# Optimization experiments

Measured on AMD Instinct MI355X. Metric: run time of the kernel, lower is better.

## Reference

```python
import jax, jax.numpy as jnp
import numpy as np

N_NODES = 100000
N_EDGES = 1600000


def spmm(edge_index, edge_vals, x, n_nodes):
    # adj @ x with adj in COO form: out[dst] += val * x[src]
    src = edge_index[0]
    dst = edge_index[1]
    gathered = x[src] * edge_vals[:, None]  # [E, F]
    return jax.ops.segment_sum(gathered, dst, num_segments=n_nodes)


def setup_inputs() -> dict:
    key = jax.random.key(0)
    ks = jax.random.split(key, 8)
    x = jax.random.normal(ks[0], (N_NODES, 512), dtype=jnp.float32)
    edge_index = jax.random.randint(ks[1], (2, N_EDGES), 0, N_NODES, dtype=jnp.int64)
    edge_vals = jax.random.uniform(ks[2], (N_EDGES,), dtype=jnp.float32)
    # xavier-uniform style weights, zero biases (as in initialize_weights)
    def xavier(k, fan_in, fan_out):
        lim = float(np.sqrt(6.0 / (fan_in + fan_out)))
        return jax.random.uniform(k, (fan_in, fan_out), minval=-lim, maxval=lim, dtype=jnp.float32)
    W1 = xavier(ks[3], 512, 128)
    b1 = jnp.zeros((128,), jnp.float32)
    W2 = xavier(ks[4], 128, 64)
    b2 = jnp.zeros((64,), jnp.float32)
    W3 = xavier(ks[5], 64, 16)
    b3 = jnp.zeros((16,), jnp.float32)
    return {"x": x, "edge_index": edge_index, "edge_vals": edge_vals,
            "W1": W1, "b1": b1, "W2": W2, "b2": b2, "W3": W3, "b3": b3}


def reference(x, edge_index, edge_vals, W1, b1, W2, b2, W3, b3):
    n = x.shape[0]
    h = jax.nn.relu(spmm(edge_index, edge_vals, x @ W1 + b1, n))
    h = jax.nn.relu(spmm(edge_index, edge_vals, h @ W2 + b2, n))
    logits = spmm(edge_index, edge_vals, h @ W3 + b3, n)
    logp = jax.nn.log_softmax(logits, axis=1)
    return jnp.argmax(logp, axis=1)
```

## Files before the change

### kernel.cpp

```cpp
#include <hip/hip_runtime.h>

typedef _Float16 half8 __attribute__((ext_vector_type(8)));
typedef float floatx4 __attribute__((ext_vector_type(4)));

#define BSHIFT 7
#define BMASK 127
#define EPB 8192
#define P2CAP 4096

__device__ __forceinline__ void g2lds16(const void* g, void* l) {
    __builtin_amdgcn_global_load_lds(
        (const __attribute__((address_space(1))) void*)(unsigned long long)g,
        (__attribute__((address_space(3))) void*)(unsigned int)(unsigned long long)l,
        16, 0, 0);
}


__global__ __launch_bounds__(256) void p1a_hist(const int* __restrict__ dst,
                                                int* __restrict__ hist,
                                                int E, int NBUCK) {
    extern __shared__ int lh[];
    int b = blockIdx.x, t = threadIdx.x;
    for (int k = t; k < NBUCK; k += 256) lh[k] = 0;
    __syncthreads();
    int e0 = b * EPB;
    int eend = min(e0 + EPB, E);
    for (int i = e0 + t; i < eend; i += 256)
        atomicAdd(&lh[dst[i] >> BSHIFT], 1);
    __syncthreads();
    for (int k = t; k < NBUCK; k += 256) hist[(size_t)b * NBUCK + k] = lh[k];
}

__global__ __launch_bounds__(256) void p1b_scan(const int* __restrict__ hist,
                                                int* __restrict__ blockOff,
                                                int* __restrict__ btot,
                                                int NBLK, int NBUCK) {
    int k = blockIdx.x * 256 + threadIdx.x;
    if (k < NBUCK) {
        int run = 0;
        for (int b = 0; b < NBLK; ++b) {
            int c = hist[(size_t)b * NBUCK + k];
            blockOff[(size_t)b * NBUCK + k] = run;
            run += c;
        }
        btot[k] = run;
    }
}

__global__ __launch_bounds__(1024) void p1c_bscan(const int* __restrict__ btot,
                                                  int* __restrict__ bstart,
                                                  int* __restrict__ rowptr,
                                                  int NBUCK, int M, int E) {
    __shared__ int s[1024];
    int tid = threadIdx.x;
    int v = (tid < NBUCK) ? btot[tid] : 0;
    s[tid] = v;
    __syncthreads();
    for (int off = 1; off < 1024; off <<= 1) {
        int t = (tid >= off) ? s[tid - off] : 0;
        __syncthreads();
        s[tid] += t;
        __syncthreads();
    }
    if (tid < NBUCK) bstart[tid] = s[tid] - v;
    if (tid == 0) rowptr[M] = E;
}

__global__ __launch_bounds__(256) void p1d_scatter(const int* __restrict__ src,
                                                   const int* __restrict__ dst,
                                                   const float* __restrict__ val,
                                                   const int* __restrict__ bstart,
                                                   const int* __restrict__ blockOff,
                                                   int2* __restrict__ tmp,
                                                   int E, int NBUCK) {
    extern __shared__ int cur[];
    int b = blockIdx.x, t = threadIdx.x;
    for (int k = t; k < NBUCK; k += 256)
        cur[k] = bstart[k] + blockOff[(size_t)b * NBUCK + k];
    __syncthreads();
    int e0 = b * EPB;
    int eend = min(e0 + EPB, E);
    for (int i = e0 + t; i < eend; i += 256) {
        int d = dst[i];
        int p = atomicAdd(&cur[d >> BSHIFT], 1);
        int2 pk;
        pk.x = src[i] | ((d & BMASK) << 20);
        pk.y = __float_as_int(val[i]);
        tmp[p] = pk;
    }
}

__global__ __launch_bounds__(256) void p2_sort(const int2* __restrict__ tmp,
                                               const int* __restrict__ bstart,
                                               const int* __restrict__ btot,
                                               int* __restrict__ rowptr,
                                               int2* __restrict__ ssv, int M) {
    __shared__ int2 ebuf[P2CAP];
    __shared__ int h[128], sc[128], curs[128];
    int k = blockIdx.x, t = threadIdx.x;
    int base = bstart[k], n = btot[k];
    for (int j = t; j < 128; j += 256) h[j] = 0;
    __syncthreads();
    int nl = min(n, P2CAP);
    for (int i = t; i < nl; i += 256) {
        int2 e = tmp[base + i];
        ebuf[i] = e;
        atomicAdd(&h[e.x >> 20], 1);
    }
    for (int i = P2CAP + t; i < n; i += 256) {
        int2 e = tmp[base + i];
        atomicAdd(&h[e.x >> 20], 1);
    }
    __syncthreads();
    if (t < 128) sc[t] = h[t];
    __syncthreads();
    for (int off = 1; off < 128; off <<= 1) {
        int v = (t < 128 && t >= off) ? sc[t - off] : 0;
        __syncthreads();
        if (t < 128) sc[t] += v;
        __syncthreads();
    }
    if (t < 128) {
        int node = (k << BSHIFT) + t;
        int excl = sc[t] - h[t];
        if (node < M) rowptr[node] = base + excl;
        curs[t] = excl;
    }
    __syncthreads();
    for (int i = t; i < nl; i += 256) {
        int2 e = ebuf[i];
        int p = atomicAdd(&curs[e.x >> 20], 1);
        int2 o; o.x = e.x & 0xFFFFF; o.y = e.y;
        ssv[base + p] = o;
    }
    for (int i = P2CAP + t; i < n; i += 256) {
        int2 e = tmp[base + i];
        int p = atomicAdd(&curs[e.x >> 20], 1);
        int2 o; o.x = e.x & 0xFFFFF; o.y = e.y;
        ssv[base + p] = o;
    }
}


__global__ __launch_bounds__(256) void prep_w1(const float* __restrict__ W1,
                                               _Float16* __restrict__ Whi,
                                               _Float16* __restrict__ Wlo) {
    int tid = blockIdx.x * 256 + threadIdx.x;
    int n = tid >> 9;
    int k = tid & 511;
    float w = W1[(size_t)k * 128 + n];
    _Float16 h = (_Float16)w;
    Whi[tid] = h;
    Wlo[tid] = (_Float16)(w - (float)h);
}

__global__ __launch_bounds__(256) void prep_w2(const float* __restrict__ W2,
                                               _Float16* __restrict__ Whi,
                                               _Float16* __restrict__ Wlo) {
    int tid = blockIdx.x * 256 + threadIdx.x;
    int n = tid >> 7;
    int k = tid & 127;
    float w = W2[(size_t)k * 64 + n];
    _Float16 h = (_Float16)w;
    Whi[tid] = h;
    Wlo[tid] = (_Float16)(w - (float)h);
}

__device__ __forceinline__ void split8(float4 f0, float4 f1, half8& h, half8& l) {
    float f[8] = {f0.x, f0.y, f0.z, f0.w, f1.x, f1.y, f1.z, f1.w};
#pragma unroll
    for (int j = 0; j < 8; ++j) {
        _Float16 hi = (_Float16)f[j];
        h[j] = hi;
        l[j] = (_Float16)(f[j] - (float)hi);
    }
}


__global__ __launch_bounds__(256) void gemm1_mfma(const float* __restrict__ X,
                                                  const _Float16* __restrict__ Whi,
                                                  const _Float16* __restrict__ Wlo,
                                                  const float* __restrict__ bias,
                                                  float* __restrict__ out, int M) {
    __shared__ char smem[2 * 16384];
    int t = threadIdx.x;
    int w = t >> 6;
    int lane = t & 63;
    int quad = lane >> 4;
    int l16 = lane & 15;
    int bm = blockIdx.x * 128;
    int m0 = bm + w * 32;

    int ra0 = min(m0 + l16, M - 1);
    int ra1 = min(m0 + 16 + l16, M - 1);
    const float* a0p = X + (size_t)ra0 * 512 + quad * 8;
    const float* a1p = X + (size_t)ra1 * 512 + quad * 8;

    int chunk0 = w * 4;
    const _Float16* gsrc[4];
#pragma unroll
    for (int c = 0; c < 4; ++c) {
        int idx = (chunk0 + c) * 1024 + lane * 16;
        int sec = idx >> 13;
        int row = (idx & 8191) >> 6;
        int kch = (idx >> 4) & 3;
        gsrc[c] = (sec ? Wlo : Whi) + (size_t)row * 512 + kch * 8;
    }
#pragma unroll
    for (int c = 0; c < 4; ++c)
        g2lds16(gsrc[c], smem + (chunk0 + c) * 1024);
    float4 af00 = *(const float4*)(a0p);
    float4 af01 = *(const float4*)(a0p + 4);
    float4 af10 = *(const float4*)(a1p);
    float4 af11 = *(const float4*)(a1p + 4);

    floatx4 acc[2][8];
#pragma unroll
    for (int mt = 0; mt < 2; ++mt)
#pragma unroll
        for (int nt = 0; nt < 8; ++nt) acc[mt][nt] = (floatx4){0.f, 0.f, 0.f, 0.f};

    for (int i = 0; i < 16; ++i) {
        int k0 = i * 32;
        __syncthreads();
        if (i < 15) {
            char* nbuf = smem + ((i + 1) & 1) * 16384;
#pragma unroll
            for (int c = 0; c < 4; ++c)
                g2lds16(gsrc[c] + k0 + 32, nbuf + (chunk0 + c) * 1024);
        }
        float4 nf00 = af00, nf01 = af01, nf10 = af10, nf11 = af11;
        if (i < 15) {
            nf00 = *(const float4*)(a0p + k0 + 32);
            nf01 = *(const float4*)(a0p + k0 + 36);
            nf10 = *(const float4*)(a1p + k0 + 32);
            nf11 = *(const float4*)(a1p + k0 + 36);
        }
        const char* buf = smem + (i & 1) * 16384;
        half8 bh[8], bl[8];
#pragma unroll
        for (int nt = 0; nt < 8; ++nt) {
            int off = (nt * 16 + l16) * 64 + quad * 16;
            bh[nt] = *(const half8*)(buf + off);
            bl[nt] = *(const half8*)(buf + 8192 + off);
        }
        half8 ah0, al0, ah1, al1;
        split8(af00, af01, ah0, al0);
        split8(af10, af11, ah1, al1);
#pragma unroll
        for (int nt = 0; nt < 8; ++nt) {
            acc[0][nt] = __builtin_amdgcn_mfma_f32_16x16x32_f16(ah0, bh[nt], acc[0][nt], 0, 0, 0);
            acc[1][nt] = __builtin_amdgcn_mfma_f32_16x16x32_f16(ah1, bh[nt], acc[1][nt], 0, 0, 0);
            acc[0][nt] = __builtin_amdgcn_mfma_f32_16x16x32_f16(ah0, bl[nt], acc[0][nt], 0, 0, 0);
            acc[1][nt] = __builtin_amdgcn_mfma_f32_16x16x32_f16(ah1, bl[nt], acc[1][nt], 0, 0, 0);
            acc[0][nt] = __builtin_amdgcn_mfma_f32_16x16x32_f16(al0, bh[nt], acc[0][nt], 0, 0, 0);
            acc[1][nt] = __builtin_amdgcn_mfma_f32_16x16x32_f16(al1, bh[nt], acc[1][nt], 0, 0, 0);
        }
        af00 = nf00; af01 = nf01; af10 = nf10; af11 = nf11;
    }

#pragma unroll
    for (int nt = 0; nt < 8; ++nt) {
        int col = nt * 16 + l16;
        float bv = bias[col];
#pragma unroll
        for (int mt = 0; mt < 2; ++mt)
#pragma unroll
            for (int r = 0; r < 4; ++r) {
                int row = m0 + mt * 16 + quad * 4 + r;
                if (row < M) out[(size_t)row * 128 + col] = acc[mt][nt][r] + bv;
            }
    }
}


__global__ __launch_bounds__(256) void gemm2_mfma(const float* __restrict__ H,
                                                  const _Float16* __restrict__ Whi,
                                                  const _Float16* __restrict__ Wlo,
                                                  const float* __restrict__ bias,
                                                  float* __restrict__ out, int M) {
    __shared__ char smem[2 * 64 * 320];
    int t = threadIdx.x;
#pragma unroll
    for (int i = 0; i < 4; ++i) {
        int gidx = i * 256 + t;
        int row = gidx >> 4, col = gidx & 15;
        *(float4*)(smem + row * 320 + col * 16) = ((const float4*)Whi)[gidx];
        *(float4*)(smem + 20480 + row * 320 + col * 16) = ((const float4*)Wlo)[gidx];
    }
    __syncthreads();

    int w = t >> 6;
    int lane = t & 63;
    int quad = lane >> 4;
    int l16 = lane & 15;
    int m0 = blockIdx.x * 128 + w * 32;
    int ra0 = min(m0 + l16, M - 1);
    int ra1 = min(m0 + 16 + l16, M - 1);
    const float* a0p = H + (size_t)ra0 * 128 + quad * 8;
    const float* a1p = H + (size_t)ra1 * 128 + quad * 8;

    floatx4 acc[2][4];
#pragma unroll
    for (int mt = 0; mt < 2; ++mt)
#pragma unroll
        for (int nt = 0; nt < 4; ++nt) acc[mt][nt] = (floatx4){0.f, 0.f, 0.f, 0.f};

#pragma unroll
    for (int k0 = 0; k0 < 128; k0 += 32) {
        float4 af00 = *(const float4*)(a0p + k0);
        float4 af01 = *(const float4*)(a0p + k0 + 4);
        float4 af10 = *(const float4*)(a1p + k0);
        float4 af11 = *(const float4*)(a1p + k0 + 4);
        af00.x = fmaxf(af00.x, 0.f); af00.y = fmaxf(af00.y, 0.f);
        af00.z = fmaxf(af00.z, 0.f); af00.w = fmaxf(af00.w, 0.f);
        af01.x = fmaxf(af01.x, 0.f); af01.y = fmaxf(af01.y, 0.f);
        af01.z = fmaxf(af01.z, 0.f); af01.w = fmaxf(af01.w, 0.f);
        af10.x = fmaxf(af10.x, 0.f); af10.y = fmaxf(af10.y, 0.f);
        af10.z = fmaxf(af10.z, 0.f); af10.w = fmaxf(af10.w, 0.f);
        af11.x = fmaxf(af11.x, 0.f); af11.y = fmaxf(af11.y, 0.f);
        af11.z = fmaxf(af11.z, 0.f); af11.w = fmaxf(af11.w, 0.f);
        half8 bh[4], bl[4];
#pragma unroll
        for (int nt = 0; nt < 4; ++nt) {
            int off = (nt * 16 + l16) * 320 + k0 * 2 + quad * 16;
            bh[nt] = *(const half8*)(smem + off);
            bl[nt] = *(const half8*)(smem + 20480 + off);
        }
        half8 ah0, al0, ah1, al1;
        split8(af00, af01, ah0, al0);
        split8(af10, af11, ah1, al1);
#pragma unroll
        for (int nt = 0; nt < 4; ++nt) {
            acc[0][nt] = __builtin_amdgcn_mfma_f32_16x16x32_f16(ah0, bh[nt], acc[0][nt], 0, 0, 0);
            acc[1][nt] = __builtin_amdgcn_mfma_f32_16x16x32_f16(ah1, bh[nt], acc[1][nt], 0, 0, 0);
            acc[0][nt] = __builtin_amdgcn_mfma_f32_16x16x32_f16(ah0, bl[nt], acc[0][nt], 0, 0, 0);
            acc[1][nt] = __builtin_amdgcn_mfma_f32_16x16x32_f16(ah1, bl[nt], acc[1][nt], 0, 0, 0);
            acc[0][nt] = __builtin_amdgcn_mfma_f32_16x16x32_f16(al0, bh[nt], acc[0][nt], 0, 0, 0);
            acc[1][nt] = __builtin_amdgcn_mfma_f32_16x16x32_f16(al1, bh[nt], acc[1][nt], 0, 0, 0);
        }
    }

#pragma unroll
    for (int nt = 0; nt < 4; ++nt) {
        int col = nt * 16 + l16;
        float bv = bias[col];
#pragma unroll
        for (int mt = 0; mt < 2; ++mt)
#pragma unroll
            for (int r = 0; r < 4; ++r) {
                int row = m0 + mt * 16 + quad * 4 + r;
                if (row < M) out[(size_t)row * 64 + col] = acc[mt][nt][r] + bv;
            }
    }
}


__global__ __launch_bounds__(256) void gemm3(const float* __restrict__ H,
                                             const float* __restrict__ W,
                                             const float* __restrict__ bias,
                                             float* __restrict__ out, int M) {
    __shared__ float Ws[64 * 16];
    __shared__ float Xs[32 * 68];
    int t = threadIdx.x;
    int m0 = blockIdx.x * 32;
    ((float4*)Ws)[t] = ((const float4*)W)[t];
#pragma unroll
    for (int i = 0; i < 2; i++) {
        int idx = t + i * 256;
        int gi = idx * 4;
        int row = gi >> 6, col = gi & 63;
        float4 v = make_float4(0.f, 0.f, 0.f, 0.f);
        if (m0 + row < M) v = *(const float4*)(H + (size_t)(m0 + row) * 64 + col);
        v.x = fmaxf(v.x, 0.f); v.y = fmaxf(v.y, 0.f);
        v.z = fmaxf(v.z, 0.f); v.w = fmaxf(v.w, 0.f);
        *(float4*)&Xs[row * 68 + col] = v;
    }
    __syncthreads();
    int node = t >> 3;
    int j = t & 7;
    float a0 = 0.f, a1 = 0.f;
#pragma unroll 8
    for (int k = 0; k < 64; ++k) {
        float xv = Xs[node * 68 + k];
        a0 += xv * Ws[k * 16 + j * 2];
        a1 += xv * Ws[k * 16 + j * 2 + 1];
    }
    int row = m0 + node;
    if (row < M) {
        a0 += bias[j * 2];
        a1 += bias[j * 2 + 1];
        float2 r = make_float2(a0, a1);
        *(float2*)(out + (size_t)row * 16 + j * 2) = r;
    }
}


__global__ __launch_bounds__(256) void spmm128(const int* __restrict__ rowptr,
                                               const int2* __restrict__ ssv,
                                               const float* __restrict__ T,
                                               float* __restrict__ H, int N) {
    int lane = threadIdx.x & 63;
    int node = __builtin_amdgcn_readfirstlane(blockIdx.x * 4 + (threadIdx.x >> 6));
    if (node >= N) return;
    int beg = rowptr[node], end = rowptr[node + 1];
    float a0 = 0.f, a1 = 0.f;
    int i = beg;
    int n4 = beg + ((end - beg) & ~3);
    for (; i < n4; i += 4) {
        int2 e0 = ssv[i], e1 = ssv[i + 1], e2 = ssv[i + 2], e3 = ssv[i + 3];
        const float* p0 = T + (size_t)e0.x * 128;
        const float* p1 = T + (size_t)e1.x * 128;
        const float* p2 = T + (size_t)e2.x * 128;
        const float* p3 = T + (size_t)e3.x * 128;
        float x0 = p0[lane], y0 = p0[lane + 64];
        float x1 = p1[lane], y1 = p1[lane + 64];
        float x2 = p2[lane], y2 = p2[lane + 64];
        float x3 = p3[lane], y3 = p3[lane + 64];
        float v0 = __int_as_float(e0.y), v1 = __int_as_float(e1.y);
        float v2 = __int_as_float(e2.y), v3 = __int_as_float(e3.y);
        a0 += v0 * x0; a1 += v0 * y0;
        a0 += v1 * x1; a1 += v1 * y1;
        a0 += v2 * x2; a1 += v2 * y2;
        a0 += v3 * x3; a1 += v3 * y3;
    }
    for (; i < end; ++i) {
        int2 e = ssv[i];
        float v = __int_as_float(e.y);
        const float* p = T + (size_t)e.x * 128;
        a0 += v * p[lane];
        a1 += v * p[lane + 64];
    }
    float* o = H + (size_t)node * 128;
    o[lane] = a0;
    o[lane + 64] = a1;
}

__global__ __launch_bounds__(256) void spmm64(const int* __restrict__ rowptr,
                                              const int2* __restrict__ ssv,
                                              const float* __restrict__ T,
                                              float* __restrict__ H, int N) {
    int lane = threadIdx.x & 63;
    int node = __builtin_amdgcn_readfirstlane(blockIdx.x * 4 + (threadIdx.x >> 6));
    if (node >= N) return;
    int beg = rowptr[node], end = rowptr[node + 1];
    float a = 0.f;
    int i = beg;
    int n4 = beg + ((end - beg) & ~3);
    for (; i < n4; i += 4) {
        int2 e0 = ssv[i], e1 = ssv[i + 1], e2 = ssv[i + 2], e3 = ssv[i + 3];
        float x0 = T[(size_t)e0.x * 64 + lane];
        float x1 = T[(size_t)e1.x * 64 + lane];
        float x2 = T[(size_t)e2.x * 64 + lane];
        float x3 = T[(size_t)e3.x * 64 + lane];
        a += __int_as_float(e0.y) * x0;
        a += __int_as_float(e1.y) * x1;
        a += __int_as_float(e2.y) * x2;
        a += __int_as_float(e3.y) * x3;
    }
    for (; i < end; ++i) {
        int2 e = ssv[i];
        a += __int_as_float(e.y) * T[(size_t)e.x * 64 + lane];
    }
    H[(size_t)node * 64 + lane] = a;
}

__global__ __launch_bounds__(256) void spmm_argmax(const int* __restrict__ rowptr,
                                                   const int2* __restrict__ ssv,
                                                   const float* __restrict__ T,
                                                   int* __restrict__ out, int N) {
    int lane = threadIdx.x & 63;
    int wave = threadIdx.x >> 6;
    int sub = lane >> 4;
    int fl = lane & 15;
    int node = blockIdx.x * 16 + wave * 4 + sub;
    float acc = 0.f;
    if (node < N) {
        int beg = rowptr[node], end = rowptr[node + 1];
        int i = beg;
        int n4 = beg + ((end - beg) & ~3);
        for (; i < n4; i += 4) {
            int2 e0 = ssv[i], e1 = ssv[i + 1], e2 = ssv[i + 2], e3 = ssv[i + 3];
            float x0 = T[(size_t)e0.x * 16 + fl];
            float x1 = T[(size_t)e1.x * 16 + fl];
            float x2 = T[(size_t)e2.x * 16 + fl];
            float x3 = T[(size_t)e3.x * 16 + fl];
            acc += __int_as_float(e0.y) * x0;
            acc += __int_as_float(e1.y) * x1;
            acc += __int_as_float(e2.y) * x2;
            acc += __int_as_float(e3.y) * x3;
        }
        for (; i < end; ++i) {
            int2 e = ssv[i];
            acc += __int_as_float(e.y) * T[(size_t)e.x * 16 + fl];
        }
    }
    float bv = acc;
    int bi = fl;
#pragma unroll
    for (int off = 8; off >= 1; off >>= 1) {
        float ov = __shfl_xor(bv, off, 64);
        int oi = __shfl_xor(bi, off, 64);
        if (ov > bv || (ov == bv && oi < bi)) { bv = ov; bi = oi; }
    }
    if (node < N && fl == 0) out[node] = bi;
}


extern "C" void kernel_launch(void* const* d_in, const int* in_sizes, int n_in,
                              void* d_out, int out_size, void* d_ws, size_t ws_size,
                              hipStream_t stream) {
    const float* x  = (const float*)d_in[0];
    const int*   ei = (const int*)d_in[1];
    const float* ev = (const float*)d_in[2];
    const float* W1 = (const float*)d_in[3];
    const float* b1 = (const float*)d_in[4];
    const float* W2 = (const float*)d_in[5];
    const float* b2 = (const float*)d_in[6];
    const float* W3 = (const float*)d_in[7];
    const float* b3 = (const float*)d_in[8];
    int* out = (int*)d_out;

    int M = in_sizes[0] / 512;
    int E = in_sizes[2];
    const int* src = ei;
    const int* dst = ei + E;

    int NBUCK = (M + BMASK) >> BSHIFT;
    int NBLK  = (E + EPB - 1) / EPB;

    char* ws = (char*)d_ws;
    size_t off = 0;
    auto alloc = [&](size_t bytes) {
        size_t o = off;
        off += (bytes + 255) & ~(size_t)255;
        return o;
    };
    float*    tA      = (float*)(ws + alloc((size_t)M * 128 * 4));
    float*    hB      = (float*)(ws + alloc((size_t)M * 128 * 4));
    int2*     ssv     = (int2*) (ws + alloc((size_t)E * 8));
    int*      rowptr  = (int*)  (ws + alloc((size_t)(M + 1) * 4));
    int*      hist    = (int*)  (ws + alloc((size_t)NBLK * NBUCK * 4));
    int*      blockOff= (int*)  (ws + alloc((size_t)NBLK * NBUCK * 4));
    int*      btot    = (int*)  (ws + alloc((size_t)NBUCK * 4));
    int*      bstart  = (int*)  (ws + alloc((size_t)NBUCK * 4));
    _Float16* w1hi    = (_Float16*)(ws + alloc(512 * 128 * 2));
    _Float16* w1lo    = (_Float16*)(ws + alloc(512 * 128 * 2));
    _Float16* w2hi    = (_Float16*)(ws + alloc(128 * 64 * 2));
    _Float16* w2lo    = (_Float16*)(ws + alloc(128 * 64 * 2));
    int2*     tmp     = (int2*)hB;

    prep_w1<<<256, 256, 0, stream>>>(W1, w1hi, w1lo);
    prep_w2<<<32, 256, 0, stream>>>(W2, w2hi, w2lo);
    p1a_hist<<<NBLK, 256, NBUCK * 4, stream>>>(dst, hist, E, NBUCK);
    p1b_scan<<<(NBUCK + 255) / 256, 256, 0, stream>>>(hist, blockOff, btot, NBLK, NBUCK);
    p1c_bscan<<<1, 1024, 0, stream>>>(btot, bstart, rowptr, NBUCK, M, E);
    p1d_scatter<<<NBLK, 256, NBUCK * 4, stream>>>(src, dst, ev, bstart, blockOff, tmp, E, NBUCK);
    p2_sort<<<NBUCK, 256, 0, stream>>>(tmp, bstart, btot, rowptr, ssv, M);

    gemm1_mfma<<<(M + 127) / 128, 256, 0, stream>>>(x, w1hi, w1lo, b1, tA, M);
    spmm128<<<(M + 3) / 4, 256, 0, stream>>>(rowptr, ssv, tA, hB, M);
    gemm2_mfma<<<(M + 127) / 128, 256, 0, stream>>>(hB, w2hi, w2lo, b2, tA, M);
    spmm64<<<(M + 3) / 4, 256, 0, stream>>>(rowptr, ssv, tA, hB, M);
    gemm3<<<(M + 31) / 32, 256, 0, stream>>>(hB, W3, b3, tA, M);
    spmm_argmax<<<(M + 15) / 16, 256, 0, stream>>>(rowptr, ssv, tA, out, M);
}
```

Before: 695.2 us.

## Vectorize SpMM gathers with float4 edge-parallel lanes and fuse scan kernels

The three SpMM kernels now read feature rows as float4. Lanes are split across several edges at once, with shuffle-xor reductions to combine the partial sums, which gives wider memory transactions and more edges in flight per wave. The argmax kernel now uses 4 threads per node, each holding 4 features, so each block covers 64 nodes. The two scan kernels are merged into a single one-block launch, which removes one launch but serializes the bucket scan onto that block. The change adds shuffle overhead and tail masking, and the order of floating-point summation changes.

New measurement: 687.3 us. Within noise of the previous version (-1.1%).

```diff
diff --git a/kernel.cpp b/kernel.cpp
--- a/kernel.cpp
+++ b/kernel.cpp
@@ -31,13 +31,16 @@
     for (int k = t; k < NBUCK; k += 256) hist[(size_t)b * NBUCK + k] = lh[k];
 }
 
-__global__ __launch_bounds__(256) void p1b_scan(const int* __restrict__ hist,
-                                                int* __restrict__ blockOff,
-                                                int* __restrict__ btot,
-                                                int NBLK, int NBUCK) {
-    int k = blockIdx.x * 256 + threadIdx.x;
+__global__ __launch_bounds__(1024) void p1bc(const int* __restrict__ hist,
+                                             int* __restrict__ blockOff,
+                                             int* __restrict__ btot,
+                                             int* __restrict__ bstart,
+                                             int* __restrict__ rowptr,
+                                             int NBLK, int NBUCK, int M, int E) {
+    __shared__ int s[1024];
+    int k = threadIdx.x;
+    int run = 0;
     if (k < NBUCK) {
-        int run = 0;
         for (int b = 0; b < NBLK; ++b) {
             int c = hist[(size_t)b * NBUCK + k];
             blockOff[(size_t)b * NBUCK + k] = run;
@@ -45,25 +48,16 @@
         }
         btot[k] = run;
     }
-}
-
-__global__ __launch_bounds__(1024) void p1c_bscan(const int* __restrict__ btot,
-                                                  int* __restrict__ bstart,
-                                                  int* __restrict__ rowptr,
-                                                  int NBUCK, int M, int E) {
-    __shared__ int s[1024];
-    int tid = threadIdx.x;
-    int v = (tid < NBUCK) ? btot[tid] : 0;
-    s[tid] = v;
+    s[k] = (k < NBUCK) ? run : 0;
     __syncthreads();
     for (int off = 1; off < 1024; off <<= 1) {
-        int t = (tid >= off) ? s[tid - off] : 0;
+        int v = (k >= off) ? s[k - off] : 0;
         __syncthreads();
-        s[tid] += t;
+        s[k] += v;
         __syncthreads();
     }
-    if (tid < NBUCK) bstart[tid] = s[tid] - v;
-    if (tid == 0) rowptr[M] = E;
+    if (k < NBUCK) bstart[k] = s[k] - run;
+    if (k == 0) rowptr[M] = E;
 }
 
 __global__ __launch_bounds__(256) void p1d_scatter(const int* __restrict__ src,
@@ -404,36 +398,43 @@
     int node = __builtin_amdgcn_readfirstlane(blockIdx.x * 4 + (threadIdx.x >> 6));
     if (node >= N) return;
     int beg = rowptr[node], end = rowptr[node + 1];
-    float a0 = 0.f, a1 = 0.f;
+    int half = lane >> 5;
+    int c4 = (lane & 31) << 2;
+    float4 acc = make_float4(0.f, 0.f, 0.f, 0.f);
     int i = beg;
-    int n4 = beg + ((end - beg) & ~3);
-    for (; i < n4; i += 4) {
-        int2 e0 = ssv[i], e1 = ssv[i + 1], e2 = ssv[i + 2], e3 = ssv[i + 3];
-        const float* p0 = T + (size_t)e0.x * 128;
-        const float* p1 = T + (size_t)e1.x * 128;
-        const float* p2 = T + (size_t)e2.x * 128;
-        const float* p3 = T + (size_t)e3.x * 128;
-        float x0 = p0[lane], y0 = p0[lane + 64];
-        float x1 = p1[lane], y1 = p1[lane + 64];
-        float x2 = p2[lane], y2 = p2[lane + 64];
-        float x3 = p3[lane], y3 = p3[lane + 64];
-        float v0 = __int_as_float(e0.y), v1 = __int_as_float(e1.y);
-        float v2 = __int_as_float(e2.y), v3 = __int_as_float(e3.y);
-        a0 += v0 * x0; a1 += v0 * y0;
-        a0 += v1 * x1; a1 += v1 * y1;
-        a0 += v2 * x2; a1 += v2 * y2;
-        a0 += v3 * x3; a1 += v3 * y3;
-    }
-    for (; i < end; ++i) {
+    int cnt = end - beg;
+    int n8 = beg + (cnt & ~7);
+    for (; i < n8; i += 8) {
+#pragma unroll
+        for (int u = 0; u < 4; ++u) {
+            int2 e = ssv[i + 2 * u + half];
+            float v = __int_as_float(e.y);
+            float4 xv = *(const float4*)(T + ((size_t)e.x << 7) + c4);
+            acc.x += v * xv.x; acc.y += v * xv.y;
+            acc.z += v * xv.z; acc.w += v * xv.w;
+        }
+    }
+    int n2 = beg + (cnt & ~1);
+    for (; i < n2; i += 2) {
+        int2 e = ssv[i + half];
+        float v = __int_as_float(e.y);
+        float4 xv = *(const float4*)(T + ((size_t)e.x << 7) + c4);
+        acc.x += v * xv.x; acc.y += v * xv.y;
+        acc.z += v * xv.z; acc.w += v * xv.w;
+    }
+    if (i < end) {
         int2 e = ssv[i];
-        float v = __int_as_float(e.y);
-        const float* p = T + (size_t)e.x * 128;
-        a0 += v * p[lane];
-        a1 += v * p[lane + 64];
-    }
-    float* o = H + (size_t)node * 128;
-    o[lane] = a0;
-    o[lane + 64] = a1;
+        float v = half ? 0.f : __int_as_float(e.y);
+        float4 xv = *(const float4*)(T + ((size_t)e.x << 7) + c4);
+        acc.x += v * xv.x; acc.y += v * xv.y;
+        acc.z += v * xv.z; acc.w += v * xv.w;
+    }
+    acc.x += __shfl_xor(acc.x, 32, 64);
+    acc.y += __shfl_xor(acc.y, 32, 64);
+    acc.z += __shfl_xor(acc.z, 32, 64);
+    acc.w += __shfl_xor(acc.w, 32, 64);
+    if (half == 0)
+        *(float4*)(H + ((size_t)node << 7) + c4) = acc;
 }
 
 __global__ __launch_bounds__(256) void spmm64(const int* __restrict__ rowptr,
@@ -444,66 +445,92 @@
     int node = __builtin_amdgcn_readfirstlane(blockIdx.x * 4 + (threadIdx.x >> 6));
     if (node >= N) return;
     int beg = rowptr[node], end = rowptr[node + 1];
-    float a = 0.f;
+    int es = lane >> 4;
+    int c4 = (lane & 15) << 2;
+    float4 acc = make_float4(0.f, 0.f, 0.f, 0.f);
     int i = beg;
-    int n4 = beg + ((end - beg) & ~3);
+    int cnt = end - beg;
+    int n8 = beg + (cnt & ~7);
+    for (; i < n8; i += 8) {
+#pragma unroll
+        for (int u = 0; u < 2; ++u) {
+            int2 e = ssv[i + 4 * u + es];
+            float v = __int_as_float(e.y);
+            float4 xv = *(const float4*)(T + ((size_t)e.x << 6) + c4);
+            acc.x += v * xv.x; acc.y += v * xv.y;
+            acc.z += v * xv.z; acc.w += v * xv.w;
+        }
+    }
+    int n4 = beg + (cnt & ~3);
     for (; i < n4; i += 4) {
-        int2 e0 = ssv[i], e1 = ssv[i + 1], e2 = ssv[i + 2], e3 = ssv[i + 3];
-        float x0 = T[(size_t)e0.x * 64 + lane];
-        float x1 = T[(size_t)e1.x * 64 + lane];
-        float x2 = T[(size_t)e2.x * 64 + lane];
-        float x3 = T[(size_t)e3.x * 64 + lane];
-        a += __int_as_float(e0.y) * x0;
-        a += __int_as_float(e1.y) * x1;
-        a += __int_as_float(e2.y) * x2;
-        a += __int_as_float(e3.y) * x3;
-    }
-    for (; i < end; ++i) {
-        int2 e = ssv[i];
-        a += __int_as_float(e.y) * T[(size_t)e.x * 64 + lane];
-    }
-    H[(size_t)node * 64 + lane] = a;
+        int2 e = ssv[i + es];
+        float v = __int_as_float(e.y);
+        float4 xv = *(const float4*)(T + ((size_t)e.x << 6) + c4);
+        acc.x += v * xv.x; acc.y += v * xv.y;
+        acc.z += v * xv.z; acc.w += v * xv.w;
+    }
+    if (i < end) {
+        int idx = i + es;
+        int2 e = ssv[idx < end ? idx : i];
+        float v = (idx < end) ? __int_as_float(e.y) : 0.f;
+        float4 xv = *(const float4*)(T + ((size_t)e.x << 6) + c4);
+        acc.x += v * xv.x; acc.y += v * xv.y;
+        acc.z += v * xv.z; acc.w += v * xv.w;
+    }
+    acc.x += __shfl_xor(acc.x, 16, 64);
+    acc.y += __shfl_xor(acc.y, 16, 64);
+    acc.z += __shfl_xor(acc.z, 16, 64);
+    acc.w += __shfl_xor(acc.w, 16, 64);
+    acc.x += __shfl_xor(acc.x, 32, 64);
+    acc.y += __shfl_xor(acc.y, 32, 64);
+    acc.z += __shfl_xor(acc.z, 32, 64);
+    acc.w += __shfl_xor(acc.w, 32, 64);
+    if (lane < 16)
+        *(float4*)(H + ((size_t)node << 6) + c4) = acc;
 }
 
 __global__ __launch_bounds__(256) void spmm_argmax(const int* __restrict__ rowptr,
                                                    const int2* __restrict__ ssv,
                                                    const float* __restrict__ T,
                                                    int* __restrict__ out, int N) {
-    int lane = threadIdx.x & 63;
-    int wave = threadIdx.x >> 6;
-    int sub = lane >> 4;
-    int fl = lane & 15;
-    int node = blockIdx.x * 16 + wave * 4 + sub;
-    float acc = 0.f;
-    if (node < N) {
-        int beg = rowptr[node], end = rowptr[node + 1];
-        int i = beg;
-        int n4 = beg + ((end - beg) & ~3);
-        for (; i < n4; i += 4) {
-            int2 e0 = ssv[i], e1 = ssv[i + 1], e2 = ssv[i + 2], e3 = ssv[i + 3];
-            float x0 = T[(size_t)e0.x * 16 + fl];
-            float x1 = T[(size_t)e1.x * 16 + fl];
-            float x2 = T[(size_t)e2.x * 16 + fl];
-            float x3 = T[(size_t)e3.x * 16 + fl];
-            acc += __int_as_float(e0.y) * x0;
-            acc += __int_as_float(e1.y) * x1;
-            acc += __int_as_float(e2.y) * x2;
-            acc += __int_as_float(e3.y) * x3;
-        }
-        for (; i < end; ++i) {
-            int2 e = ssv[i];
-            acc += __int_as_float(e.y) * T[(size_t)e.x * 16 + fl];
-        }
-    }
-    float bv = acc;
-    int bi = fl;
-#pragma unroll
-    for (int off = 8; off >= 1; off >>= 1) {
+    int t = threadIdx.x;
+    int node = blockIdx.x * 64 + (t >> 2);
+    int q = t & 3;
+    int c4 = q << 2;
+    int beg = 0, end = 0;
+    if (node < N) { beg = rowptr[node]; end = rowptr[node + 1]; }
+    float4 acc = make_float4(0.f, 0.f, 0.f, 0.f);
+    int i = beg;
+    int cnt = end - beg;
+    int n4 = beg + (cnt & ~3);
+    for (; i < n4; i += 4) {
+#pragma unroll
+        for (int u = 0; u < 4; ++u) {
+            int2 e = ssv[i + u];
+            float v = __int_as_float(e.y);
+            float4 xv = *(const float4*)(T + ((size_t)e.x << 4) + c4);
+            acc.x += v * xv.x; acc.y += v * xv.y;
+            acc.z += v * xv.z; acc.w += v * xv.w;
+        }
+    }
+    for (; i < end; ++i) {
+        int2 e = ssv[i];
+        float v = __int_as_float(e.y);
+        float4 xv = *(const float4*)(T + ((size_t)e.x << 4) + c4);
+        acc.x += v * xv.x; acc.y += v * xv.y;
+        acc.z += v * xv.z; acc.w += v * xv.w;
+    }
+    float bv = acc.x; int bi = c4;
+    if (acc.y > bv) { bv = acc.y; bi = c4 + 1; }
+    if (acc.z > bv) { bv = acc.z; bi = c4 + 2; }
+    if (acc.w > bv) { bv = acc.w; bi = c4 + 3; }
+#pragma unroll
+    for (int off = 1; off <= 2; off <<= 1) {
         float ov = __shfl_xor(bv, off, 64);
         int oi = __shfl_xor(bi, off, 64);
         if (ov > bv || (ov == bv && oi < bi)) { bv = ov; bi = oi; }
     }
-    if (node < N && fl == 0) out[node] = bi;
+    if (node < N && q == 0) out[node] = bi;
 }
 
 
@@ -553,8 +580,7 @@
     prep_w1<<<256, 256, 0, stream>>>(W1, w1hi, w1lo);
     prep_w2<<<32, 256, 0, stream>>>(W2, w2hi, w2lo);
     p1a_hist<<<NBLK, 256, NBUCK * 4, stream>>>(dst, hist, E, NBUCK);
-    p1b_scan<<<(NBUCK + 255) / 256, 256, 0, stream>>>(hist, blockOff, btot, NBLK, NBUCK);
-    p1c_bscan<<<1, 1024, 0, stream>>>(btot, bstart, rowptr, NBUCK, M, E);
+    p1bc<<<1, 1024, 0, stream>>>(hist, blockOff, btot, bstart, rowptr, NBLK, NBUCK, M, E);
     p1d_scatter<<<NBLK, 256, NBUCK * 4, stream>>>(src, dst, ev, bstart, blockOff, tmp, E, NBUCK);
     p2_sort<<<NBUCK, 256, 0, stream>>>(tmp, bstart, btot, rowptr, ssv, M);
 
@@ -563,5 +589,5 @@
     gemm2_mfma<<<(M + 127) / 128, 256, 0, stream>>>(hB, w2hi, w2lo, b2, tA, M);
     spmm64<<<(M + 3) / 4, 256, 0, stream>>>(rowptr, ssv, tA, hB, M);
     gemm3<<<(M + 31) / 32, 256, 0, stream>>>(hB, W3, b3, tA, M);
-    spmm_argmax<<<(M + 15) / 16, 256, 0, stream>>>(rowptr, ssv, tA, out, M);
-}
+    spmm_argmax<<<(M + 63) / 64, 256, 0, stream>>>(rowptr, ssv, tA, out, M);
+}
```
